# Kernel optimization log

Hardware: AMD Instinct MI355X
Metric: run time of the kernel (lower is better)

## Reference

```python
import jax, jax.numpy as jnp
import numpy as np

B, S, E, OUT = 16, 2048, 256, 256


def setup_inputs() -> dict:
    key = jax.random.key(0)
    k1, k2 = jax.random.split(key)
    x = jax.random.normal(k1, (B, S, E), dtype=jnp.float32)
    alpha = jnp.float32(0.5)  # nn.Parameter(torch.tensor(0.5))
    W = jax.random.normal(k2, (OUT, E), dtype=jnp.float32) * (1.0 / np.sqrt(E))
    b = jnp.zeros((OUT,), dtype=jnp.float32)
    return {"x": x, "alpha\u0308".replace("\u0308", ""): alpha, "W": W, "b": b}


def reference(x, alpha, W, b):
    # Gaussian energy-well self-attention: q = k = v = x, shape (B, S, E)
    # cdist(q, k, p=2)**2 == ||q||^2 + ||k||^2 - 2 q.k
    sq = jnp.sum(x * x, axis=-1)                                   # (B, S)
    d2 = sq[:, :, None] + sq[:, None, :] - 2.0 * jnp.einsum(
        "bse,bte->bst", x, x)                                      # (B, S, S)
    d2 = jnp.maximum(d2, 0.0)
    weights = jnp.exp(-alpha * d2)                                 # (B, S, S)
    weights = jax.nn.softmax(weights, axis=-1)
    attn = jnp.einsum("bst,bte->bse", weights, x)                  # (B, S, E)
    pooled = attn.mean(axis=1)                                     # (B, E)
    return pooled @ W.T + b                                        # (B, OUT)
```

## Files before the change

kernel.cpp:

```cpp
#include <hip/hip_runtime.h>
#include <hip/hip_bf16.h>

#define NB 16
#define NS 2048
#define NE 256
#define NOUT 256
#define CAP 49152
#define RCAP 384

typedef __attribute__((ext_vector_type(4))) float f32x4;
typedef __attribute__((ext_vector_type(8))) short s16x8;
typedef __attribute__((ext_vector_type(4))) short s16x4;
typedef unsigned int u32;
typedef unsigned long long u64;

__device__ __forceinline__ short bf16rn(float f) {
  unsigned u = __builtin_bit_cast(unsigned, f);
  u += 0x7FFFu + ((u >> 16) & 1u);
  return (short)(u >> 16);
}
__device__ __forceinline__ float bf16f(short s) {
  unsigned u = ((unsigned)(unsigned short)s) << 16;
  return __builtin_bit_cast(float, u);
}
__device__ __forceinline__ void gld_lds16(const void* g, void* l) {
  __builtin_amdgcn_global_load_lds(
      (const __attribute__((address_space(1))) u32*)g,
      (__attribute__((address_space(3))) u32*)l, 16, 0, 0);
}

__global__ __launch_bounds__(256) void prep_kernel(const float* __restrict__ x,
                                                   short* __restrict__ xbf,
                                                   float* __restrict__ sq,
                                                   u32* __restrict__ counter) {
  if (blockIdx.x == 0 && threadIdx.x == 0) *counter = 0u;
  int row = blockIdx.x * 4 + (threadIdx.x >> 6);
  int lane = threadIdx.x & 63;
  f32x4 v = *(const f32x4*)(x + (size_t)row * NE + lane * 4);
  s16x4 p;
  p[0] = bf16rn(v.x); p[1] = bf16rn(v.y); p[2] = bf16rn(v.z); p[3] = bf16rn(v.w);
  *(s16x4*)(xbf + (size_t)row * NE + lane * 4) = p;
  float s = v.x * v.x + v.y * v.y + v.z * v.z + v.w * v.w;
#pragma unroll
  for (int off = 32; off; off >>= 1) s += __shfl_xor(s, off);
  if (lane == 0) sq[row] = s;
}

template <int KH>
__device__ __forceinline__ void compute_half(const char* buf, int lrow, int lq,
                                             const s16x8 (&af)[2][8],
                                             f32x4 (&acc)[2][8]) {
#pragma unroll
  for (int ks = 0; ks < 4; ++ks) {
    s16x8 bv[8];
#pragma unroll
    for (int n = 0; n < 8; ++n) {
      int col = n * 16 + lrow;
      bv[n] = *(const s16x8*)(buf + (ks >> 1) * 16384 + col * 128 +
                              (((ks & 1) * 64 + lq * 16) ^ ((col & 7) << 4)));
    }
#pragma unroll
    for (int m = 0; m < 2; ++m)
#pragma unroll
      for (int n = 0; n < 8; ++n)
        acc[m][n] = __builtin_amdgcn_mfma_f32_16x16x32_bf16(
            af[m][KH * 4 + ks], bv[n], acc[m][n], 0, 0, 0);
  }
}

__global__ __launch_bounds__(256, 2) void gram_kernel(
    const short* __restrict__ xbf, const float* __restrict__ sqg,
    const float* __restrict__ alpha_p, float* __restrict__ rpart,
    u32* __restrict__ counter, u32* __restrict__ records) {
  __shared__ __align__(16) char smem[73728];
  __shared__ u32 rec_meta[RCAP];
  __shared__ float rec_e[RCAP];
  __shared__ u32 rec_cnt, rec_gbase;
  float* sqall = (float*)(smem + 65536);

  const int tid = threadIdx.x;
  const int lane = tid & 63;
  const int wid = tid >> 6;
  const int lrow = lane & 15, lq = lane >> 4;

  const int nbid = (blockIdx.x & 7) * 64 + (blockIdx.x >> 3);
  const int b = nbid >> 5;
  const int strip = (nbid >> 1) & 15;
  const int half = nbid & 1;
  const int rowbase = strip * 128;
  const char* xc = (const char*)(xbf + (size_t)b * NS * NE);
  const float alpha = alpha_p[0];
  const float nal = -alpha;
  const float thresh = 17.328680f / alpha;

  if (tid == 0) rec_cnt = 0u;

  {
    const f32x4* s4 = (const f32x4*)(sqg + b * NS);
    f32x4 a0 = s4[tid * 2], a1 = s4[tid * 2 + 1];
    *(f32x4*)&sqall[tid * 8] = a0;
    *(f32x4*)&sqall[tid * 8 + 4] = a1;
  }
#pragma unroll
  for (int c = 0; c < 16; ++c) {
    int rl = wid * 32 + c * 2 + (lane >> 5);
    int inner = ((lane & 31) * 16) ^ ((rl & 7) << 4);
    gld_lds16(xc + (size_t)(rowbase + rl) * 512 + inner,
              smem + wid * 16384 + c * 1024 + lane * 16);
  }
  __syncthreads();

  s16x8 af[2][8];
#pragma unroll
  for (int m = 0; m < 2; ++m) {
    int row = wid * 32 + m * 16 + lrow;
#pragma unroll
    for (int ks = 0; ks < 8; ++ks)
      af[m][ks] = *(const s16x8*)(smem + row * 512 +
                                  ((ks * 64 + lq * 16) ^ ((row & 7) << 4)));
  }
  float rr[2][4], minrr = 3.4e38f;
#pragma unroll
  for (int m = 0; m < 2; ++m)
#pragma unroll
    for (int j = 0; j < 4; ++j) {
      rr[m][j] = sqall[rowbase + wid * 32 + m * 16 + lq * 4 + j];
      minrr = fminf(minrr, rr[m][j]);
    }
  __syncthreads();

  const int swzl = ((lane & 7) * 16) ^ ((lane >> 3) << 4);
  auto stageB = [&](int bt, int kh, char* buf) {
    const char* base = xc + (size_t)(half * 8 + bt) * 65536 + kh * 256 +
                       (wid >> 1) * 128 + swzl;
    char* dst = buf + wid * 8192 + lane * 16;
#pragma unroll
    for (int i = 0; i < 8; ++i) {
      int colOff = (wid & 1) * 64 + i * 8 + (lane >> 3);
      gld_lds16(base + (size_t)colOff * 512, dst + i * 1024);
    }
  };

  f32x4 acc[2][8];
#pragma unroll
  for (int m = 0; m < 2; ++m)
#pragma unroll
    for (int n = 0; n < 8; ++n) acc[m][n] = (f32x4){0.f, 0.f, 0.f, 0.f};
  float prs[2][4] = {{0.f, 0.f, 0.f, 0.f}, {0.f, 0.f, 0.f, 0.f}};

  stageB(0, 0, smem);
  __syncthreads();

#pragma unroll 1
  for (int bt = 0; bt < 8; ++bt) {
    stageB(bt, 1, smem + 32768);
    compute_half<0>(smem, lrow, lq, af, acc);
    __syncthreads();
    if (bt < 7) stageB(bt + 1, 0, smem);
    compute_half<1>(smem + 32768, lrow, lq, af, acc);

    {
      const int btg = half * 8 + bt;
      float cc[8], mincc = 3.4e38f;
#pragma unroll
      for (int n = 0; n < 8; ++n) {
        cc[n] = sqall[btg * 128 + n * 16 + lrow];
        mincc = fminf(mincc, cc[n]);
      }
      float maxg = -3.4e38f;
#pragma unroll
      for (int m = 0; m < 2; ++m)
#pragma unroll
        for (int n = 0; n < 8; ++n)
#pragma unroll
          for (int j = 0; j < 4; ++j) maxg = fmaxf(maxg, acc[m][n][j]);
      bool fast = (minrr + mincc - 2.f * maxg > thresh);
      if (__all(fast)) {
#pragma unroll
        for (int m = 0; m < 2; ++m)
#pragma unroll
          for (int j = 0; j < 4; ++j) prs[m][j] += 8.0f;
      } else {
#pragma unroll
        for (int m = 0; m < 2; ++m) {
#pragma unroll
          for (int j = 0; j < 4; ++j) {
            float rj = rr[m][j];
#pragma unroll
            for (int n = 0; n < 8; ++n) {
              float d2 = fmaxf(fmaf(-2.f, acc[m][n][j], rj + cc[n]), 0.f);
              float w0 = __expf(nal * d2);
              float e = __expf(w0);
              prs[m][j] += e;
              if (d2 < thresh) {
                u32 idx = atomicAdd(&rec_cnt, 1u);
                if (idx < RCAP) {
                  int srow = rowbase + wid * 32 + m * 16 + lq * 4 + j;
                  int tcol = btg * 128 + n * 16 + lrow;
                  rec_meta[idx] = ((u32)srow << 11) | (u32)tcol;
                  rec_e[idx] = e;
                }
              }
            }
          }
        }
      }
#pragma unroll
      for (int m = 0; m < 2; ++m)
#pragma unroll
        for (int n = 0; n < 8; ++n) acc[m][n] = (f32x4){0.f, 0.f, 0.f, 0.f};
    }
    __syncthreads();
  }

#pragma unroll
  for (int m = 0; m < 2; ++m)
#pragma unroll
    for (int j = 0; j < 4; ++j) {
      float v = prs[m][j];
      v += __shfl_xor(v, 1);
      v += __shfl_xor(v, 2);
      v += __shfl_xor(v, 4);
      v += __shfl_xor(v, 8);
      if (lrow == 0)
        rpart[(size_t)(b * 2 + half) * NS + rowbase + wid * 32 + m * 16 +
              lq * 4 + j] = v;
    }

  __syncthreads();
  u32 cnt = rec_cnt;
  if (cnt > RCAP) cnt = RCAP;
  if (cnt) {
    if (tid == 0) rec_gbase = atomicAdd(counter, cnt);
    __syncthreads();
    u32 gb = rec_gbase;
    for (u32 i = tid; i < cnt; i += 256) {
      u32 g = gb + i;
      if (g < CAP) {
        records[2 * g] = ((u32)b << 22) | rec_meta[i];
        records[2 * g + 1] = __builtin_bit_cast(u32, rec_e[i]);
      }
    }
  }
}

__global__ __launch_bounds__(512) void finale_kernel(
    const short* __restrict__ xbf, const float* __restrict__ rpart,
    const u32* __restrict__ counter, const u32* __restrict__ records,
    const float* __restrict__ W, const float* __restrict__ bias,
    float* __restrict__ out) {
  __shared__ float rinv_l[NS];
  __shared__ float c_l[NS];
  __shared__ float red[16 * 256];
  __shared__ float pooled_l[NE];
  const int b = blockIdx.x;
  const int tid = threadIdx.x;
  const int lane = tid & 63;
  const int wv = tid >> 6;

  float inv_acc = 0.f;
#pragma unroll
  for (int k = 0; k < 4; ++k) {
    int row = k * 512 + tid;
    float r = rpart[(size_t)(2 * b) * NS + row] +
              rpart[(size_t)(2 * b + 1) * NS + row];
    float inv = 1.0f / r;
    rinv_l[row] = inv;
    inv_acc += inv;
  }
#pragma unroll
  for (int off = 32; off; off >>= 1) inv_acc += __shfl_xor(inv_acc, off);
  if (lane == 0) red[wv] = inv_acc;
  __syncthreads();
  float tot = 0.f;
#pragma unroll
  for (int g = 0; g < 8; ++g) tot += red[g];
#pragma unroll
  for (int k = 0; k < 4; ++k) c_l[k * 512 + tid] = tot;
  __syncthreads();

  u32 cnt = *counter;
  if (cnt > CAP) cnt = CAP;
  for (u32 i = tid; i < cnt; i += 512) {
    u32 meta = records[2 * i];
    if ((int)(meta >> 22) != b) continue;
    float e = __builtin_bit_cast(float, records[2 * i + 1]);
    int s = (meta >> 11) & 2047, t = meta & 2047;
    atomicAdd(&c_l[t], (e - 1.0f) * rinv_l[s]);
  }
  __syncthreads();

  const short* xb = xbf + (size_t)b * NS * NE;
  const int e8 = (lane & 31) * 8;
  const int tgrp = wv * 2 + (lane >> 5);
  float acc[8] = {0.f, 0.f, 0.f, 0.f, 0.f, 0.f, 0.f, 0.f};
#pragma unroll 4
  for (int tt = 0; tt < 128; ++tt) {
    int t = tgrp * 128 + tt;
    float cv = c_l[t];
    s16x8 v = *(const s16x8*)(xb + (size_t)t * NE + e8);
#pragma unroll
    for (int j = 0; j < 8; ++j) acc[j] = fmaf(cv, bf16f(v[j]), acc[j]);
  }
#pragma unroll
  for (int j = 0; j < 8; ++j) red[tgrp * 256 + e8 + j] = acc[j];
  __syncthreads();
  if (tid < NE) {
    float s = 0.f;
#pragma unroll
    for (int g = 0; g < 16; ++g) s += red[g * 256 + tid];
    pooled_l[tid] = s * (1.0f / NS);
  }
  __syncthreads();

  if (tid < NOUT) {
    const f32x4* wr4 = (const f32x4*)(W + (size_t)tid * NE);
    float a = bias[tid];
#pragma unroll 8
    for (int e = 0; e < 64; ++e) {
      f32x4 w4 = wr4[e];
      a += pooled_l[e * 4 + 0] * w4.x + pooled_l[e * 4 + 1] * w4.y +
           pooled_l[e * 4 + 2] * w4.z + pooled_l[e * 4 + 3] * w4.w;
    }
    out[b * NOUT + tid] = a;
  }
}

extern "C" void kernel_launch(void* const* d_in, const int* in_sizes, int n_in,
                              void* d_out, int out_size, void* d_ws, size_t ws_size,
                              hipStream_t stream) {
  const float* x = (const float*)d_in[0];
  const float* alpha = (const float*)d_in[1];
  const float* W = (const float*)d_in[2];
  const float* bias = (const float*)d_in[3];
  float* out = (float*)d_out;

  u32* counter = (u32*)d_ws;
  float* sq = (float*)(counter + 32);
  float* rpart = sq + NB * NS;
  u32* records = (u32*)(rpart + 2 * NB * NS);
  short* xbf = (short*)(records + 2 * CAP);

  prep_kernel<<<NB * NS / 4, 256, 0, stream>>>(x, xbf, sq, counter);
  gram_kernel<<<512, 256, 0, stream>>>(xbf, sq, alpha, rpart, counter, records);
  finale_kernel<<<NB, 512, 0, stream>>>(xbf, rpart, counter, records, W, bias,
                                        out);
}
```

Before: 157.2 us.

## Split gram work into column quarters, shrink LDS staging, widen finale block

The gram kernel now splits each row strip's columns into four quarters instead of two, doubling the grid to 1024 blocks. It loads A fragments and squared norms straight from global memory instead of staging them in LDS, and double-buffers smaller 16KB B chunks with a barrier per chunk. Shared memory per block drops sharply, which should allow more resident blocks and better latency hiding. The cost is more barriers, redundant global A loads per block, and four partial row sums that the finale kernel must combine, now with 1024 threads per block.

```diff
diff --git a/kernel.cpp b/kernel.cpp
--- a/kernel.cpp
+++ b/kernel.cpp
@@ -46,48 +46,26 @@
   if (lane == 0) sq[row] = s;
 }
 
-template <int KH>
-__device__ __forceinline__ void compute_half(const char* buf, int lrow, int lq,
-                                             const s16x8 (&af)[2][8],
-                                             f32x4 (&acc)[2][8]) {
-#pragma unroll
-  for (int ks = 0; ks < 4; ++ks) {
-    s16x8 bv[8];
-#pragma unroll
-    for (int n = 0; n < 8; ++n) {
-      int col = n * 16 + lrow;
-      bv[n] = *(const s16x8*)(buf + (ks >> 1) * 16384 + col * 128 +
-                              (((ks & 1) * 64 + lq * 16) ^ ((col & 7) << 4)));
-    }
-#pragma unroll
-    for (int m = 0; m < 2; ++m)
-#pragma unroll
-      for (int n = 0; n < 8; ++n)
-        acc[m][n] = __builtin_amdgcn_mfma_f32_16x16x32_bf16(
-            af[m][KH * 4 + ks], bv[n], acc[m][n], 0, 0, 0);
-  }
-}
-
 __global__ __launch_bounds__(256, 2) void gram_kernel(
     const short* __restrict__ xbf, const float* __restrict__ sqg,
     const float* __restrict__ alpha_p, float* __restrict__ rpart,
     u32* __restrict__ counter, u32* __restrict__ records) {
-  __shared__ __align__(16) char smem[73728];
+  __shared__ __align__(16) char smem[32768];
   __shared__ u32 rec_meta[RCAP];
   __shared__ float rec_e[RCAP];
   __shared__ u32 rec_cnt, rec_gbase;
-  float* sqall = (float*)(smem + 65536);
 
   const int tid = threadIdx.x;
   const int lane = tid & 63;
   const int wid = tid >> 6;
   const int lrow = lane & 15, lq = lane >> 4;
 
-  const int nbid = (blockIdx.x & 7) * 64 + (blockIdx.x >> 3);
-  const int b = nbid >> 5;
-  const int strip = (nbid >> 1) & 15;
-  const int half = nbid & 1;
+  const int nbid = (blockIdx.x & 7) * 128 + (blockIdx.x >> 3);
+  const int b = nbid >> 6;
+  const int strip = (nbid >> 2) & 15;
+  const int quad = nbid & 3;
   const int rowbase = strip * 128;
+  const int colbase = quad * 512;
   const char* xc = (const char*)(xbf + (size_t)b * NS * NE);
   const float alpha = alpha_p[0];
   const float nal = -alpha;
@@ -95,49 +73,31 @@
 
   if (tid == 0) rec_cnt = 0u;
 
-  {
-    const f32x4* s4 = (const f32x4*)(sqg + b * NS);
-    f32x4 a0 = s4[tid * 2], a1 = s4[tid * 2 + 1];
-    *(f32x4*)&sqall[tid * 8] = a0;
-    *(f32x4*)&sqall[tid * 8 + 4] = a1;
-  }
-#pragma unroll
-  for (int c = 0; c < 16; ++c) {
-    int rl = wid * 32 + c * 2 + (lane >> 5);
-    int inner = ((lane & 31) * 16) ^ ((rl & 7) << 4);
-    gld_lds16(xc + (size_t)(rowbase + rl) * 512 + inner,
-              smem + wid * 16384 + c * 1024 + lane * 16);
-  }
-  __syncthreads();
-
   s16x8 af[2][8];
 #pragma unroll
   for (int m = 0; m < 2; ++m) {
-    int row = wid * 32 + m * 16 + lrow;
+    const char* arow = xc + (size_t)(rowbase + wid * 32 + m * 16 + lrow) * 512;
 #pragma unroll
     for (int ks = 0; ks < 8; ++ks)
-      af[m][ks] = *(const s16x8*)(smem + row * 512 +
-                                  ((ks * 64 + lq * 16) ^ ((row & 7) << 4)));
+      af[m][ks] = *(const s16x8*)(arow + ks * 64 + lq * 16);
   }
   float rr[2][4], minrr = 3.4e38f;
 #pragma unroll
   for (int m = 0; m < 2; ++m)
 #pragma unroll
     for (int j = 0; j < 4; ++j) {
-      rr[m][j] = sqall[rowbase + wid * 32 + m * 16 + lq * 4 + j];
+      rr[m][j] = sqg[b * NS + rowbase + wid * 32 + m * 16 + lq * 4 + j];
       minrr = fminf(minrr, rr[m][j]);
     }
-  __syncthreads();
 
   const int swzl = ((lane & 7) * 16) ^ ((lane >> 3) << 4);
-  auto stageB = [&](int bt, int kh, char* buf) {
-    const char* base = xc + (size_t)(half * 8 + bt) * 65536 + kh * 256 +
-                       (wid >> 1) * 128 + swzl;
-    char* dst = buf + wid * 8192 + lane * 16;
-#pragma unroll
-    for (int i = 0; i < 8; ++i) {
-      int colOff = (wid & 1) * 64 + i * 8 + (lane >> 3);
-      gld_lds16(base + (size_t)colOff * 512, dst + i * 1024);
+  auto stageB = [&](int bt, int c, char* buf) {
+    const char* base = xc + (size_t)(colbase + bt * 128 + wid * 32 + (lane >> 3)) * 512 +
+                       c * 128 + swzl;
+    char* dst = buf + wid * 4096 + lane * 16;
+#pragma unroll
+    for (int i = 0; i < 4; ++i) {
+      gld_lds16(base + (size_t)(i * 8) * 512, dst + i * 1024);
     }
   };
 
@@ -152,65 +112,84 @@
   __syncthreads();
 
 #pragma unroll 1
-  for (int bt = 0; bt < 8; ++bt) {
-    stageB(bt, 1, smem + 32768);
-    compute_half<0>(smem, lrow, lq, af, acc);
-    __syncthreads();
-    if (bt < 7) stageB(bt + 1, 0, smem);
-    compute_half<1>(smem + 32768, lrow, lq, af, acc);
-
-    {
-      const int btg = half * 8 + bt;
-      float cc[8], mincc = 3.4e38f;
-#pragma unroll
-      for (int n = 0; n < 8; ++n) {
-        cc[n] = sqall[btg * 128 + n * 16 + lrow];
-        mincc = fminf(mincc, cc[n]);
+  for (int bt = 0; bt < 4; ++bt) {
+#pragma unroll
+    for (int c = 0; c < 4; ++c) {
+      if (!(bt == 3 && c == 3)) {
+        int btn = (c == 3) ? bt + 1 : bt;
+        stageB(btn, (c + 1) & 3, smem + (((c + 1) & 1) ? 16384 : 0));
       }
-      float maxg = -3.4e38f;
-#pragma unroll
-      for (int m = 0; m < 2; ++m)
-#pragma unroll
-        for (int n = 0; n < 8; ++n)
-#pragma unroll
-          for (int j = 0; j < 4; ++j) maxg = fmaxf(maxg, acc[m][n][j]);
-      bool fast = (minrr + mincc - 2.f * maxg > thresh);
-      if (__all(fast)) {
+      const char* buf = smem + ((c & 1) ? 16384 : 0);
+#pragma unroll
+      for (int ks = 0; ks < 2; ++ks) {
+        s16x8 bv[8];
+#pragma unroll
+        for (int n = 0; n < 8; ++n) {
+          int col = n * 16 + lrow;
+          bv[n] = *(const s16x8*)(buf + col * 128 +
+                                  ((ks * 64 + lq * 16) ^ ((col & 7) << 4)));
+        }
 #pragma unroll
         for (int m = 0; m < 2; ++m)
 #pragma unroll
-          for (int j = 0; j < 4; ++j) prs[m][j] += 8.0f;
-      } else {
-#pragma unroll
-        for (int m = 0; m < 2; ++m) {
-#pragma unroll
-          for (int j = 0; j < 4; ++j) {
-            float rj = rr[m][j];
-#pragma unroll
-            for (int n = 0; n < 8; ++n) {
-              float d2 = fmaxf(fmaf(-2.f, acc[m][n][j], rj + cc[n]), 0.f);
-              float w0 = __expf(nal * d2);
-              float e = __expf(w0);
-              prs[m][j] += e;
-              if (d2 < thresh) {
-                u32 idx = atomicAdd(&rec_cnt, 1u);
-                if (idx < RCAP) {
-                  int srow = rowbase + wid * 32 + m * 16 + lq * 4 + j;
-                  int tcol = btg * 128 + n * 16 + lrow;
-                  rec_meta[idx] = ((u32)srow << 11) | (u32)tcol;
-                  rec_e[idx] = e;
+          for (int n = 0; n < 8; ++n)
+            acc[m][n] = __builtin_amdgcn_mfma_f32_16x16x32_bf16(
+                af[m][c * 2 + ks], bv[n], acc[m][n], 0, 0, 0);
+      }
+
+      if (c == 3) {
+        const int btg = quad * 4 + bt;
+        float cc[8], mincc = 3.4e38f;
+#pragma unroll
+        for (int n = 0; n < 8; ++n) {
+          cc[n] = sqg[b * NS + btg * 128 + n * 16 + lrow];
+          mincc = fminf(mincc, cc[n]);
+        }
+        float maxg = -3.4e38f;
+#pragma unroll
+        for (int m = 0; m < 2; ++m)
+#pragma unroll
+          for (int n = 0; n < 8; ++n)
+#pragma unroll
+            for (int j = 0; j < 4; ++j) maxg = fmaxf(maxg, acc[m][n][j]);
+        bool fast = (minrr + mincc - 2.f * maxg > thresh);
+        if (__all(fast)) {
+#pragma unroll
+          for (int m = 0; m < 2; ++m)
+#pragma unroll
+            for (int j = 0; j < 4; ++j) prs[m][j] += 8.0f;
+        } else {
+#pragma unroll
+          for (int m = 0; m < 2; ++m) {
+#pragma unroll
+            for (int j = 0; j < 4; ++j) {
+              float rj = rr[m][j];
+#pragma unroll
+              for (int n = 0; n < 8; ++n) {
+                float d2 = fmaxf(fmaf(-2.f, acc[m][n][j], rj + cc[n]), 0.f);
+                float w0 = __expf(nal * d2);
+                float e = __expf(w0);
+                prs[m][j] += e;
+                if (d2 < thresh) {
+                  u32 idx = atomicAdd(&rec_cnt, 1u);
+                  if (idx < RCAP) {
+                    int srow = rowbase + wid * 32 + m * 16 + lq * 4 + j;
+                    int tcol = btg * 128 + n * 16 + lrow;
+                    rec_meta[idx] = ((u32)srow << 11) | (u32)tcol;
+                    rec_e[idx] = e;
+                  }
                 }
               }
             }
           }
         }
+#pragma unroll
+        for (int m = 0; m < 2; ++m)
+#pragma unroll
+          for (int n = 0; n < 8; ++n) acc[m][n] = (f32x4){0.f, 0.f, 0.f, 0.f};
       }
-#pragma unroll
-      for (int m = 0; m < 2; ++m)
-#pragma unroll
-        for (int n = 0; n < 8; ++n) acc[m][n] = (f32x4){0.f, 0.f, 0.f, 0.f};
-    }
-    __syncthreads();
+      __syncthreads();
+    }
   }
 
 #pragma unroll
@@ -223,11 +202,10 @@
       v += __shfl_xor(v, 4);
       v += __shfl_xor(v, 8);
       if (lrow == 0)
-        rpart[(size_t)(b * 2 + half) * NS + rowbase + wid * 32 + m * 16 +
+        rpart[(size_t)(b * 4 + quad) * NS + rowbase + wid * 32 + m * 16 +
               lq * 4 + j] = v;
     }
 
-  __syncthreads();
   u32 cnt = rec_cnt;
   if (cnt > RCAP) cnt = RCAP;
   if (cnt) {
@@ -244,14 +222,14 @@
   }
 }
 
-__global__ __launch_bounds__(512) void finale_kernel(
+__global__ __launch_bounds__(1024) void finale_kernel(
     const short* __restrict__ xbf, const float* __restrict__ rpart,
     const u32* __restrict__ counter, const u32* __restrict__ records,
     const float* __restrict__ W, const float* __restrict__ bias,
     float* __restrict__ out) {
   __shared__ float rinv_l[NS];
   __shared__ float c_l[NS];
-  __shared__ float red[16 * 256];
+  __shared__ float red[32 * 256];
   __shared__ float pooled_l[NE];
   const int b = blockIdx.x;
   const int tid = threadIdx.x;
@@ -260,10 +238,12 @@
 
   float inv_acc = 0.f;
 #pragma unroll
-  for (int k = 0; k < 4; ++k) {
-    int row = k * 512 + tid;
-    float r = rpart[(size_t)(2 * b) * NS + row] +
-              rpart[(size_t)(2 * b + 1) * NS + row];
+  for (int k = 0; k < 2; ++k) {
+    int row = k * 1024 + tid;
+    float r = rpart[(size_t)(4 * b + 0) * NS + row] +
+              rpart[(size_t)(4 * b + 1) * NS + row] +
+              rpart[(size_t)(4 * b + 2) * NS + row] +
+              rpart[(size_t)(4 * b + 3) * NS + row];
     float inv = 1.0f / r;
     rinv_l[row] = inv;
     inv_acc += inv;
@@ -274,14 +254,14 @@
   __syncthreads();
   float tot = 0.f;
 #pragma unroll
-  for (int g = 0; g < 8; ++g) tot += red[g];
-#pragma unroll
-  for (int k = 0; k < 4; ++k) c_l[k * 512 + tid] = tot;
+  for (int g = 0; g < 16; ++g) tot += red[g];
+#pragma unroll
+  for (int k = 0; k < 2; ++k) c_l[k * 1024 + tid] = tot;
   __syncthreads();
 
   u32 cnt = *counter;
   if (cnt > CAP) cnt = CAP;
-  for (u32 i = tid; i < cnt; i += 512) {
+  for (u32 i = tid; i < cnt; i += 1024) {
     u32 meta = records[2 * i];
     if ((int)(meta >> 22) != b) continue;
     float e = __builtin_bit_cast(float, records[2 * i + 1]);
@@ -295,8 +275,8 @@
   const int tgrp = wv * 2 + (lane >> 5);
   float acc[8] = {0.f, 0.f, 0.f, 0.f, 0.f, 0.f, 0.f, 0.f};
 #pragma unroll 4
-  for (int tt = 0; tt < 128; ++tt) {
-    int t = tgrp * 128 + tt;
+  for (int tt = 0; tt < 64; ++tt) {
+    int t = tgrp * 64 + tt;
     float cv = c_l[t];
     s16x8 v = *(const s16x8*)(xb + (size_t)t * NE + e8);
 #pragma unroll
@@ -308,7 +288,7 @@
   if (tid < NE) {
     float s = 0.f;
 #pragma unroll
-    for (int g = 0; g < 16; ++g) s += red[g * 256 + tid];
+    for (int g = 0; g < 32; ++g) s += red[g * 256 + tid];
     pooled_l[tid] = s * (1.0f / NS);
   }
   __syncthreads();
@@ -338,11 +318,11 @@
   u32* counter = (u32*)d_ws;
   float* sq = (float*)(counter + 32);
   float* rpart = sq + NB * NS;
-  u32* records = (u32*)(rpart + 2 * NB * NS);
+  u32* records = (u32*)(rpart + 4 * NB * NS);
   short* xbf = (short*)(records + 2 * CAP);
 
   prep_kernel<<<NB * NS / 4, 256, 0, stream>>>(x, xbf, sq, counter);
-  gram_kernel<<<512, 256, 0, stream>>>(xbf, sq, alpha, rpart, counter, records);
-  finale_kernel<<<NB, 512, 0, stream>>>(xbf, rpart, counter, records, W, bias,
-                                        out);
-}
+  gram_kernel<<<1024, 256, 0, stream>>>(xbf, sq, alpha, rpart, counter, records);
+  finale_kernel<<<NB, 1024, 0, stream>>>(xbf, rpart, counter, records, W, bias,
+                                         out);
+}
```

After: 154.9 us. About the same (-1.5%).
